# Optimization experiments

Hardware: AMD Instinct MI355X
Metric: run time of the kernel (lower is better)

## Reference

```python
import jax, jax.numpy as jnp
import numpy as np

N, D, H, E = 4096, 256, 8, 131072
HD = D // H
EPS = 1e-5


def layernorm(x, g, b):
    mu = jnp.mean(x, axis=-1, keepdims=True)
    var = jnp.mean((x - mu) ** 2, axis=-1, keepdims=True)
    return (x - mu) * jax.lax.rsqrt(var + EPS) * g + b


def setup_inputs() -> dict:
    key = jax.random.key(0)
    ks = jax.random.split(key, 20)
    s = 1.0 / np.sqrt(D)
    x = jax.random.normal(ks[0], (N, D), jnp.float32)
    adj = jax.random.uniform(ks[1], (N, N)) < 0.01
    adj_mask = adj | jnp.eye(N, dtype=bool)  # self-loops keep softmax rows finite
    edge_index = jax.random.randint(ks[2], (2, E), 0, N, dtype=jnp.int64)
    edge_attr = jax.random.normal(ks[3], (E, D), jnp.float32)
    p = {
        'wq': jax.random.normal(ks[4], (D, D)) * s, 'bq': jnp.zeros((D,)),
        'wk': jax.random.normal(ks[5], (D, D)) * s, 'bk': jnp.zeros((D,)),
        'wv': jax.random.normal(ks[6], (D, D)) * s, 'bv': jnp.zeros((D,)),
        'wo': jax.random.normal(ks[7], (D, D)) * s, 'bo': jnp.zeros((D,)),
        'we': jax.random.normal(ks[8], (D, H)) * s, 'be': jnp.zeros((H,)),
        'w1': jax.random.normal(ks[9], (D, 4 * D)) * s, 'b1': jnp.zeros((4 * D,)),
        'w2': jax.random.normal(ks[10], (4 * D, D)) * (1.0 / np.sqrt(4 * D)), 'b2': jnp.zeros((D,)),
        'g1': jnp.ones((D,)), 'beta1': jnp.zeros((D,)),
        'g2': jnp.ones((D,)), 'beta2': jnp.zeros((D,)),
    }
    return dict(x=x, adj_mask=adj_mask, edge_index=edge_index, edge_attr=edge_attr, **p)


def reference(x, adj_mask, edge_index, edge_attr, wq, bq, wk, bk, wv, bv, wo, bo,
              we, be, w1, b1, w2, b2, g1, beta1, g2, beta2):
    n = x.shape[0]
    Q = (x @ wq + bq).reshape(n, H, HD)
    K = (x @ wk + bk).reshape(n, H, HD)
    V = (x @ wv + bv).reshape(n, H, HD)
    scores = jnp.einsum('nhd,mhd->nmh', Q, K) / np.sqrt(HD)  # [N,N,H]
    edge_bias = edge_attr @ we + be                          # [E,H]
    scores = scores.at[edge_index[0], edge_index[1]].add(edge_bias)
    s = jnp.transpose(scores, (0, 2, 1))                     # [N,H,N]
    s = jnp.where(adj_mask[:, None, :], s, -jnp.inf)
    attn = jax.nn.softmax(s, axis=-1)                        # dropout eval-mode no-op
    ctx = jnp.einsum('nhm,mhd->nhd', attn, V).reshape(n, D)
    attn_out = ctx @ wo + bo
    x1 = layernorm(x + attn_out, g1, beta1)
    ff = jax.nn.gelu(x1 @ w1 + b1, approximate=False) @ w2 + b2
    return layernorm(x1 + ff, g2, beta2)
```

## Files before the change

### kernel.cpp

```cpp
#include <hip/hip_runtime.h>
#include <math.h>

#define NN   4096
#define DD   256
#define HH   8
#define HD   32
#define DFF  1024
#define QKVW 768
#define AC   128
#define EC   128
#define SCPAD 129
#define QSP  36
#define NPB  2

typedef unsigned short ushort_t;
typedef __attribute__((ext_vector_type(8))) short short8;
typedef __attribute__((ext_vector_type(4))) float f32x4;

__device__ __forceinline__ float bf2f(unsigned short u){
  union { unsigned int i; float f; } v; v.i = ((unsigned int)u) << 16; return v.f;
}
__device__ __forceinline__ unsigned short f2bf(float f){
  union { float f; unsigned int i; } v; v.f = f;
  unsigned int x = v.i;
  return (unsigned short)((x + 0x7FFFu + ((x >> 16) & 1u)) >> 16);
}
__device__ __forceinline__ float ldf(const void* p, size_t i, int isbf){
  return isbf ? bf2f(((const ushort_t*)p)[i]) : ((const float*)p)[i];
}
__device__ __forceinline__ ushort_t ldb16(const void* p, size_t i, int isbf){
  return isbf ? ((const ushort_t*)p)[i] : f2bf(((const float*)p)[i]);
}

__global__ void k_detect(const int* __restrict__ adj32, const int* __restrict__ ei32,
                         const unsigned int* __restrict__ g1w, int* __restrict__ flags,
                         int* __restrict__ counts, int* __restrict__ cursor){
  __shared__ int c0s, c1s;
  int t = threadIdx.x;
  if (t == 0) { c0s = 0; c1s = 0; }
  __syncthreads();
  int c0 = 0, c1 = 0;
  for (int i = t; i < 960; i += 256) if (adj32[(size_t)i * 4097] != 0) c0++;
  for (int i = t; i < 2048; i += 256) if (ei32[2*i + 1] != 0) c1++;
  atomicAdd(&c0s, c0); atomicAdd(&c1s, c1);
  for (int i = t; i < NN; i += 256) { counts[i] = 0; cursor[i] = 0; }
  __syncthreads();
  if (t == 0) {
    flags[0] = (c0s == 960) ? 1 : 0;
    flags[1] = (c1s > 100) ? 1 : 0;
    flags[2] = (g1w[0] == 0x3F803F80u) ? 1 : 0;
  }
}

__global__ __launch_bounds__(256) void k_csr(const void* __restrict__ adj,
                                             const int* __restrict__ flags,
                                             int* __restrict__ alist,
                                             int* __restrict__ acnt){
  __shared__ int cntS;
  __shared__ int actS[AC];
  const int n = blockIdx.x, t = threadIdx.x;
  if (t == 0) cntS = 0;
  __syncthreads();
  if (flags[0]) {
    const uint4* arow = (const uint4*)((const int*)adj + (size_t)n * NN);
    #pragma unroll
    for (int i = 0; i < 4; i++) {
      uint4 v = arow[t + 256 * i];
      int c0 = 4 * (t + 256 * i);
      if (v.x) { int p = atomicAdd(&cntS, 1); if (p < AC) actS[p] = c0; }
      if (v.y) { int p = atomicAdd(&cntS, 1); if (p < AC) actS[p] = c0 + 1; }
      if (v.z) { int p = atomicAdd(&cntS, 1); if (p < AC) actS[p] = c0 + 2; }
      if (v.w) { int p = atomicAdd(&cntS, 1); if (p < AC) actS[p] = c0 + 3; }
    }
  } else {
    const uint4* arow = (const uint4*)((const unsigned char*)adj + (size_t)n * NN);
    uint4 v = arow[t];
    unsigned int wsv[4] = {v.x, v.y, v.z, v.w};
    #pragma unroll
    for (int q = 0; q < 4; q++) {
      unsigned int u = wsv[q];
      int c0 = 16 * t + 4 * q;
      if (u & 0x000000FFu) { int p = atomicAdd(&cntS, 1); if (p < AC) actS[p] = c0; }
      if (u & 0x0000FF00u) { int p = atomicAdd(&cntS, 1); if (p < AC) actS[p] = c0 + 1; }
      if (u & 0x00FF0000u) { int p = atomicAdd(&cntS, 1); if (p < AC) actS[p] = c0 + 2; }
      if (u & 0xFF000000u) { int p = atomicAdd(&cntS, 1); if (p < AC) actS[p] = c0 + 3; }
    }
  }
  __syncthreads();
  int m = cntS; if (m > AC) m = AC;
  if (t == 0) acnt[n] = m;
  for (int j = t; j < m; j += 256) alist[(size_t)n * AC + j] = actS[j];
}

#define NX    (NN * DD)
#define NWE   (DD * HH)
#define TPREP 768
__global__ __launch_bounds__(256) void k_prep(
    const void* __restrict__ x, const void* __restrict__ wq, const void* __restrict__ wk,
    const void* __restrict__ wv, const void* __restrict__ wo, const void* __restrict__ w1,
    const void* __restrict__ w2, const void* __restrict__ we,
    const void* __restrict__ bq, const void* __restrict__ bk, const void* __restrict__ bv,
    const void* __restrict__ bo, const void* __restrict__ be, const void* __restrict__ b1,
    const void* __restrict__ b2, const void* __restrict__ g1, const void* __restrict__ be1,
    const void* __restrict__ g2, const void* __restrict__ be2,
    const int* __restrict__ ei, const int* __restrict__ flags,
    ushort_t* __restrict__ xb,
    ushort_t* __restrict__ wqkvT, ushort_t* __restrict__ woT,
    ushort_t* __restrict__ w1T, ushort_t* __restrict__ w2T,
    float* __restrict__ wef, float* __restrict__ bqkvf,
    float* __restrict__ bof, float* __restrict__ bef,
    float* __restrict__ b1f, float* __restrict__ b2f,
    float* __restrict__ g1f, float* __restrict__ be1f,
    float* __restrict__ g2f, float* __restrict__ be2f,
    int* __restrict__ counts, int E, int TOT)
{
  const int isbf = flags[2];
  const int t = threadIdx.x;
  if (blockIdx.x < TPREP) {
    __shared__ ushort_t tile[32][36];
    int b = blockIdx.x;
    const void* src; ushort_t* dst; int R, C, ti;
    if (b < 64)       { src = wq; dst = wqkvT;              R = 256;  C = 256;  ti = b; }
    else if (b < 128) { src = wk; dst = wqkvT + 256 * 256;  R = 256;  C = 256;  ti = b - 64; }
    else if (b < 192) { src = wv; dst = wqkvT + 512 * 256;  R = 256;  C = 256;  ti = b - 128; }
    else if (b < 256) { src = wo; dst = woT;                R = 256;  C = 256;  ti = b - 192; }
    else if (b < 512) { src = w1; dst = w1T;                R = 256;  C = 1024; ti = b - 256; }
    else              { src = w2; dst = w2T;                R = 1024; C = 256;  ti = b - 512; }
    int tiles_c = C >> 5;
    int tr = ti / tiles_c, tc = ti - tr * tiles_c;
    int lr = t >> 3, lc0 = (t & 7) << 2;
    size_t sbase = (size_t)(tr * 32 + lr) * C + tc * 32 + lc0;
    if (isbf) {
      const ushort_t* s16 = (const ushort_t*)src + sbase;
      tile[lr][lc0+0] = s16[0]; tile[lr][lc0+1] = s16[1];
      tile[lr][lc0+2] = s16[2]; tile[lr][lc0+3] = s16[3];
    } else {
      const float4* sf = (const float4*)((const float*)src + sbase);
      float4 v = *sf;
      tile[lr][lc0+0] = f2bf(v.x); tile[lr][lc0+1] = f2bf(v.y);
      tile[lr][lc0+2] = f2bf(v.z); tile[lr][lc0+3] = f2bf(v.w);
    }
    __syncthreads();
    int i = t >> 3, j0 = (t & 7) << 2;
    ushort_t* dp = dst + (size_t)(tc * 32 + i) * R + tr * 32 + j0;
    ushort_t o0 = tile[j0][i], o1 = tile[j0+1][i], o2 = tile[j0+2][i], o3 = tile[j0+3][i];
    dp[0] = o0; dp[1] = o1; dp[2] = o2; dp[3] = o3;
    return;
  }
  const int ei32 = flags[1];
  const int stride = (gridDim.x - TPREP) * 256;
  for (int i = (blockIdx.x - TPREP) * 256 + t; i < TOT; i += stride) {
    int r = i;
    if (r < NX) { xb[r] = ldb16(x, r, isbf); continue; }
    r -= NX;
    if (r < E) {
      int src = ei32 ? ei[r] : ei[2 * r];
      if ((unsigned)src < (unsigned)NN) atomicAdd(&counts[src], 1);
      continue;
    }
    r -= E;
    if (r < NWE) { wef[r] = ldf(we, r, isbf); continue; }
    r -= NWE;
    if (r < QKVW) {
      const void* bs = (r < 256) ? bq : (r < 512) ? bk : bv;
      bqkvf[r] = ldf(bs, r & 255, isbf);
      continue;
    }
    r -= QKVW;
    if (r < DD)  { bof[r] = ldf(bo, r, isbf); continue; }   r -= DD;
    if (r < HH)  { bef[r] = ldf(be, r, isbf); continue; }   r -= HH;
    if (r < DFF) { b1f[r] = ldf(b1, r, isbf); continue; }   r -= DFF;
    if (r < DD)  { b2f[r] = ldf(b2, r, isbf); continue; }   r -= DD;
    if (r < DD)  { g1f[r] = ldf(g1, r, isbf); continue; }   r -= DD;
    if (r < DD)  { be1f[r] = ldf(be1, r, isbf); continue; } r -= DD;
    if (r < DD)  { g2f[r] = ldf(g2, r, isbf); continue; }   r -= DD;
    if (r < DD)  { be2f[r] = ldf(be2, r, isbf); }
  }
}

#define LDK 72
template<int BM>
__global__ __launch_bounds__(256) void k_gemm(
    const ushort_t* __restrict__ A, const ushort_t* __restrict__ Bt,
    const float* __restrict__ bias, void* __restrict__ C,
    int M, int Nn, int K, int act, int mode,
    float* __restrict__ qf, ushort_t* __restrict__ kbuf, ushort_t* __restrict__ vbuf)
{
  constexpr int NF = (BM == 64) ? 2 : 1;
  constexpr int CW = (BM == 64) ? 32 : 16;
  __shared__ ushort_t As[BM * LDK];
  __shared__ ushort_t Bs[64 * LDK];
  const int t = threadIdx.x;
  const int wave = t >> 6, lane = t & 63;
  const int l15 = lane & 15, quad = lane >> 4;
  const int wr = (BM == 64) ? (wave >> 1) : 0;
  const int wc = (BM == 64) ? (wave & 1) : wave;
  const int bm0 = blockIdx.y * BM, bn0 = blockIdx.x * 64;

  const int arow = (BM == 64) ? (t >> 2) : (t >> 3);
  const int akg  = (BM == 64) ? ((t & 3) << 4) : ((t & 7) << 3);
  const int brow = t >> 2, bkg = (t & 3) << 4;

  f32x4 acc[2][NF] = {};

  const ushort_t* ap = A  + (size_t)(bm0 + arow) * K + akg;
  const ushort_t* bp = Bt + (size_t)(bn0 + brow) * K + bkg;
  uint4 a0 = *(const uint4*)ap;
  uint4 a1{};
  if constexpr (BM == 64) a1 = *(const uint4*)(ap + 8);
  uint4 b0 = *(const uint4*)bp;
  uint4 b1 = *(const uint4*)(bp + 8);

  for (int k0 = 0; k0 < K; k0 += 64) {
    __syncthreads();
    *(uint4*)(&As[arow * LDK + akg]) = a0;
    if constexpr (BM == 64) *(uint4*)(&As[arow * LDK + akg + 8]) = a1;
    *(uint4*)(&Bs[brow * LDK + bkg]) = b0;
    *(uint4*)(&Bs[brow * LDK + bkg + 8]) = b1;
    __syncthreads();
    if (k0 + 64 < K) {
      a0 = *(const uint4*)(ap + k0 + 64);
      if constexpr (BM == 64) a1 = *(const uint4*)(ap + k0 + 64 + 8);
      b0 = *(const uint4*)(bp + k0 + 64);
      b1 = *(const uint4*)(bp + k0 + 64 + 8);
    }
    #pragma unroll
    for (int kk = 0; kk < 2; kk++) {
      short8 af[2], bf[NF];
      #pragma unroll
      for (int fr = 0; fr < 2; fr++)
        af[fr] = *(const short8*)(&As[(wr * 32 + fr * 16 + l15) * LDK + kk * 32 + quad * 8]);
      #pragma unroll
      for (int fc = 0; fc < NF; fc++)
        bf[fc] = *(const short8*)(&Bs[(wc * CW + fc * 16 + l15) * LDK + kk * 32 + quad * 8]);
      #pragma unroll
      for (int fr = 0; fr < 2; fr++)
        #pragma unroll
        for (int fc = 0; fc < NF; fc++)
          acc[fr][fc] = __builtin_amdgcn_mfma_f32_16x16x32_bf16(af[fr], bf[fc], acc[fr][fc], 0, 0, 0);
    }
  }

  #pragma unroll
  for (int fr = 0; fr < 2; fr++) {
    #pragma unroll
    for (int fc = 0; fc < NF; fc++) {
      int gn = bn0 + wc * CW + fc * 16 + l15;
      float bcol = bias[gn];
      #pragma unroll
      for (int r = 0; r < 4; r++) {
        int gm = bm0 + wr * 32 + fr * 16 + quad * 4 + r;
        float v = acc[fr][fc][r] + bcol;
        if (act) v = 0.5f * v * (1.0f + erff(v * 0.70710678118654752f));
        if (mode == 2) {
          if (gn < 256)      qf[(size_t)gm * 256 + gn] = v;
          else if (gn < 512) kbuf[(size_t)gm * 256 + (gn - 256)] = f2bf(v);
          else               vbuf[(size_t)gm * 256 + (gn - 512)] = f2bf(v);
        } else if (mode == 1) {
          ((ushort_t*)C)[(size_t)gm * Nn + gn] = f2bf(v);
        } else {
          ((float*)C)[(size_t)gm * Nn + gn] = v;
        }
      }
    }
  }
}

__global__ __launch_bounds__(256) void k_scan(const int* __restrict__ counts,
                                              int* __restrict__ off){
  __shared__ int wsum[4];
  const int t = threadIdx.x, lid = t & 63, wid = t >> 6;
  int loc[16]; int s = 0;
  #pragma unroll
  for (int j = 0; j < 16; j++) { loc[j] = counts[t * 16 + j]; s += loc[j]; }
  const int tot = s;
  #pragma unroll
  for (int o = 1; o < 64; o <<= 1) {
    int u = __shfl_up(s, o, 64);
    if (lid >= o) s += u;
  }
  if (lid == 63) wsum[wid] = s;
  __syncthreads();
  int pre = 0;
  #pragma unroll
  for (int w = 0; w < 4; w++) if (w < wid) pre += wsum[w];
  int run = pre + s - tot;
  if (t == 0) off[0] = 0;
  #pragma unroll
  for (int j = 0; j < 16; j++) { run += loc[j]; off[t * 16 + j + 1] = run; }
}

__global__ void k_scatter(const int* __restrict__ ei, const int* __restrict__ flags,
                          const int* __restrict__ off, int* __restrict__ cursor,
                          int* __restrict__ sdst, int* __restrict__ seid, int e){
  int i = blockIdx.x * 256 + threadIdx.x;
  if (i >= e) return;
  int src, dst;
  if (flags[1]) { src = ei[i];     dst = ei[e + i]; }
  else          { src = ei[2 * i]; dst = ei[2 * (e + i)]; }
  if ((unsigned)src >= (unsigned)NN) return;
  if ((unsigned)dst >= (unsigned)NN) dst = 0;
  int pos = off[src] + atomicAdd(&cursor[src], 1);
  sdst[pos] = dst; seid[pos] = i;
}

__global__ __launch_bounds__(256) void k_ebias(
    const void* __restrict__ ea, const float* __restrict__ wef,
    const float* __restrict__ bef, float* __restrict__ sbias,
    int E, const int* __restrict__ flags)
{
  __shared__ float wel[HH * DD];
  int t = threadIdx.x;
  #pragma unroll
  for (int j = 0; j < 8; j++) wel[j * DD + t] = wef[t * 8 + j];
  const int isbf = flags[2];
  __syncthreads();
  int idx = blockIdx.x * 256 + t;
  int e = idx >> 3, p = idx & 7;
  float acc[8] = {};
  if (e < E) {
    if (isbf) {
      const uint4* base = (const uint4*)((const ushort_t*)ea + (size_t)e * DD);
      #pragma unroll
      for (int q = 0; q < 4; q++) {
        uint4 u = base[q * 8 + p];
        int dbase = 64 * q + 8 * p;
        float f[8];
        union { unsigned int i; float f; } cv;
        cv.i = u.x << 16; f[0] = cv.f; cv.i = u.x & 0xFFFF0000u; f[1] = cv.f;
        cv.i = u.y << 16; f[2] = cv.f; cv.i = u.y & 0xFFFF0000u; f[3] = cv.f;
        cv.i = u.z << 16; f[4] = cv.f; cv.i = u.z & 0xFFFF0000u; f[5] = cv.f;
        cv.i = u.w << 16; f[6] = cv.f; cv.i = u.w & 0xFFFF0000u; f[7] = cv.f;
        #pragma unroll
        for (int j = 0; j < 8; j++)
          #pragma unroll
          for (int h = 0; h < 8; h++)
            acc[h] = fmaf(f[j], wel[h * DD + dbase + j], acc[h]);
      }
    } else {
      const float4* base = (const float4*)((const float*)ea + (size_t)e * DD);
      #pragma unroll
      for (int q = 0; q < 8; q++) {
        float4 u = base[q * 8 + p];
        int dbase = 32 * q + 4 * p;
        #pragma unroll
        for (int h = 0; h < 8; h++) {
          acc[h] = fmaf(u.x, wel[h * DD + dbase + 0], acc[h]);
          acc[h] = fmaf(u.y, wel[h * DD + dbase + 1], acc[h]);
          acc[h] = fmaf(u.z, wel[h * DD + dbase + 2], acc[h]);
          acc[h] = fmaf(u.w, wel[h * DD + dbase + 3], acc[h]);
        }
      }
    }
  }
  #pragma unroll
  for (int h = 0; h < 8; h++) {
    acc[h] += __shfl_xor(acc[h], 1, 8);
    acc[h] += __shfl_xor(acc[h], 2, 8);
    acc[h] += __shfl_xor(acc[h], 4, 8);
  }
  if (e < E) sbias[(size_t)e * 8 + p] = acc[p] + bef[p];
}

__global__ __launch_bounds__(256) void k_attn(
    const float* __restrict__ qf, const ushort_t* __restrict__ kb,
    const ushort_t* __restrict__ vb,
    const int* __restrict__ alist, const int* __restrict__ acnt,
    const int* __restrict__ off, const int* __restrict__ sdst,
    const int* __restrict__ seid, const float* __restrict__ sbias,
    ushort_t* __restrict__ ctxb)
{
  __shared__ float qs[NPB][HH * QSP];
  __shared__ int   act[NPB][AC];
  __shared__ float sc[NPB][HH][SCPAD];
  __shared__ int   edst[NPB][EC];
  __shared__ float ivs[NPB][HH];

  const int t = threadIdx.x;
  const int n0 = blockIdx.x * NPB;

  int na[NPB], cn[NPB], st[NPB];
  #pragma unroll
  for (int s = 0; s < NPB; s++) {
    int n = n0 + s;
    qs[s][(t >> 5) * QSP + (t & 31)] = qf[(size_t)n * DD + t];
    na[s] = min(acnt[n], AC);
    st[s] = off[n];
    int c = off[n + 1] - st[s];
    cn[s] = c < 0 ? 0 : (c > EC ? EC : c);
    for (int j = t; j < na[s]; j += 256) act[s][j] = alist[(size_t)n * AC + j];
    for (int j = t; j < cn[s]; j += 256) edst[s][j] = sdst[st[s] + j];
  }
  __syncthreads();

  #pragma unroll
  for (int s = 0; s < NPB; s++) {
    for (int item = t; item < na[s] * HH; item += 256) {
      int idx = item >> 3, h = item & 7;
      int m = act[s][idx];
      const uint4* kr = (const uint4*)(kb + (size_t)m * DD + h * HD);
      const float* qh = qs[s] + h * QSP;
      float a = 0.f;
      #pragma unroll
      for (int q4 = 0; q4 < 4; q4++) {
        uint4 u = kr[q4];
        int b = q4 * 8;
        union { unsigned int i; float f; } cv;
        cv.i = u.x << 16;         a = fmaf(cv.f, qh[b+0], a);
        cv.i = u.x & 0xFFFF0000u; a = fmaf(cv.f, qh[b+1], a);
        cv.i = u.y << 16;         a = fmaf(cv.f, qh[b+2], a);
        cv.i = u.y & 0xFFFF0000u; a = fmaf(cv.f, qh[b+3], a);
        cv.i = u.z << 16;         a = fmaf(cv.f, qh[b+4], a);
        cv.i = u.z & 0xFFFF0000u; a = fmaf(cv.f, qh[b+5], a);
        cv.i = u.w << 16;         a = fmaf(cv.f, qh[b+6], a);
        cv.i = u.w & 0xFFFF0000u; a = fmaf(cv.f, qh[b+7], a);
      }
      sc[s][h][idx] = a * 0.17677669529663687f;
    }
  }
  __syncthreads();

  #pragma unroll
  for (int s = 0; s < NPB; s++) {
    for (int item = t; item < cn[s] * HH; item += 256) {
      int j = item >> 3, h = item & 7;
      int sid = seid[st[s] + j];
      int dst = edst[s][j];
      int pos = -1;
      for (int i = 0; i < na[s]; i++) if (act[s][i] == dst) { pos = i; break; }
      if (pos >= 0) atomicAdd(&sc[s][h][pos], sbias[(size_t)sid * 8 + h]);
    }
  }
  __syncthreads();

  #pragma unroll
  for (int s = 0; s < NPB; s++) {
    const int h = t >> 5, l = t & 31;
    float lm = -1e30f;
    for (int i = l; i < na[s]; i += 32) lm = fmaxf(lm, sc[s][h][i]);
    #pragma unroll
    for (int o = 16; o > 0; o >>= 1) lm = fmaxf(lm, __shfl_down(lm, o, 32));
    lm = __shfl(lm, 0, 32);
    float ls = 0.f;
    for (int i = l; i < na[s]; i += 32) {
      float e = __expf(sc[s][h][i] - lm);
      sc[s][h][i] = e;
      ls += e;
    }
    #pragma unroll
    for (int o = 16; o > 0; o >>= 1) ls += __shfl_down(ls, o, 32);
    if (l == 0) ivs[s][h] = 1.0f / ls;
  }
  __syncthreads();

  {
    const int s_ = t >> 7, h = (t >> 4) & 7, dp = t & 15;
    const int n_a = s_ ? na[1] : na[0];
    const ushort_t* vcol = vb + h * HD + 2 * dp;
    const float* scp = sc[s_][h];
    float a0 = 0.f, a1 = 0.f;
    int i = 0;
    for (; i + 8 <= n_a; i += 8) {
      int mm[8]; unsigned int vv[8];
      #pragma unroll
      for (int u = 0; u < 8; u++) mm[u] = act[s_][i + u];
      #pragma unroll
      for (int u = 0; u < 8; u++) vv[u] = *(const unsigned int*)(vcol + (size_t)mm[u] * DD);
      #pragma unroll
      for (int u = 0; u < 8; u++) {
        float p = scp[i + u];
        a0 = fmaf(p, bf2f((ushort_t)(vv[u] & 0xFFFFu)), a0);
        a1 = fmaf(p, bf2f((ushort_t)(vv[u] >> 16)), a1);
      }
    }
    for (; i < n_a; i++) {
      unsigned int v = *(const unsigned int*)(vcol + (size_t)act[s_][i] * DD);
      float p = scp[i];
      a0 = fmaf(p, bf2f((ushort_t)(v & 0xFFFFu)), a0);
      a1 = fmaf(p, bf2f((ushort_t)(v >> 16)), a1);
    }
    float iv = ivs[s_][h];
    unsigned int ob = ((unsigned int)f2bf(a1 * iv) << 16) | (unsigned int)f2bf(a0 * iv);
    *(unsigned int*)(ctxb + (size_t)(n0 + s_) * DD + h * HD + 2 * dp) = ob;
  }
}

__global__ __launch_bounds__(256) void k_ln(
    const void* __restrict__ a, const float* __restrict__ b,
    const float* __restrict__ g, const float* __restrict__ beta,
    void* __restrict__ out, ushort_t* __restrict__ out_b,
    int a_raw, int final_mode, const int* __restrict__ flags)
{
  __shared__ float rw[4];
  __shared__ float mu_s, var_s;
  const int n = blockIdx.x, t = threadIdx.x;
  const int wid = t >> 6, lid = t & 63;
  float av = a_raw ? ldf(a, (size_t)n * DD + t, flags[2])
                   : ((const float*)a)[(size_t)n * DD + t];
  float v = av + b[(size_t)n * DD + t];
  float s = v;
  #pragma unroll
  for (int o = 32; o > 0; o >>= 1) s += __shfl_down(s, o, 64);
  if (lid == 0) rw[wid] = s;
  __syncthreads();
  if (t == 0) mu_s = (rw[0] + rw[1] + rw[2] + rw[3]) * (1.0f / 256.0f);
  __syncthreads();
  const float mu = mu_s;
  const float dv = v - mu;
  float q = dv * dv;
  #pragma unroll
  for (int o = 32; o > 0; o >>= 1) q += __shfl_down(q, o, 64);
  if (lid == 0) rw[wid] = q;
  __syncthreads();
  if (t == 0) var_s = (rw[0] + rw[1] + rw[2] + rw[3]) * (1.0f / 256.0f);
  __syncthreads();
  float res = dv * rsqrtf(var_s + 1e-5f) * g[t] + beta[t];
  if (final_mode && flags[2])
    ((ushort_t*)out)[(size_t)n * DD + t] = f2bf(res);
  else
    ((float*)out)[(size_t)n * DD + t] = res;
  if (out_b) out_b[(size_t)n * DD + t] = f2bf(res);
}

extern "C" void kernel_launch(void* const* d_in, const int* in_sizes, int n_in,
                              void* d_out, int out_size, void* d_ws, size_t ws_size,
                              hipStream_t stream)
{
  const void* x   = d_in[0];
  const void* adj = d_in[1];
  const int*  ei  = (const int*)d_in[2];
  const void* ea  = d_in[3];
  const void* wq  = d_in[4];  const void* bq  = d_in[5];
  const void* wk  = d_in[6];  const void* bk  = d_in[7];
  const void* wv  = d_in[8];  const void* bv  = d_in[9];
  const void* wo  = d_in[10]; const void* bo  = d_in[11];
  const void* we  = d_in[12]; const void* be  = d_in[13];
  const void* w1  = d_in[14]; const void* b1  = d_in[15];
  const void* w2  = d_in[16]; const void* b2  = d_in[17];
  const void* g1  = d_in[18]; const void* be1 = d_in[19];
  const void* g2  = d_in[20]; const void* be2 = d_in[21];
  const int E = in_sizes[2] / 2;

  char* w = (char*)d_ws;
  size_t o = 0;
  auto carve = [&](size_t bytes) -> void* {
    void* p = w + o; o = (o + bytes + 255) & ~(size_t)255; return p;
  };
  ushort_t* xb    = (ushort_t*)carve((size_t)NN * DD * 2);
  float*    qfb   = (float*)   carve((size_t)NN * DD * 4);
  ushort_t* kbuf  = (ushort_t*)carve((size_t)NN * DD * 2);
  ushort_t* vbuf  = (ushort_t*)carve((size_t)NN * DD * 2);
  ushort_t* wqkvT = (ushort_t*)carve((size_t)QKVW * DD * 2);
  float*    bqkvf = (float*)   carve(QKVW * 4);
  ushort_t* woT   = (ushort_t*)carve((size_t)DD * DD * 2);
  ushort_t* w1T   = (ushort_t*)carve((size_t)DFF * DD * 2);
  ushort_t* w2T   = (ushort_t*)carve((size_t)DD * DFF * 2);
  float*    wef   = (float*)   carve((size_t)DD * HH * 4);
  float*    bof   = (float*)   carve(DD * 4);
  float*    bef   = (float*)   carve(HH * 4);
  float*    b1f   = (float*)   carve(DFF * 4);
  float*    b2f   = (float*)   carve(DD * 4);
  float*    g1f   = (float*)   carve(DD * 4);
  float*    be1f  = (float*)   carve(DD * 4);
  float*    g2f   = (float*)   carve(DD * 4);
  float*    be2f  = (float*)   carve(DD * 4);
  int*      counts = (int*)carve((size_t)NN * 4);
  int*      cursor = (int*)carve((size_t)NN * 4);
  int*      off    = (int*)carve((size_t)(NN + 1) * 4);
  int*      sdst   = (int*)carve((size_t)E * 4);
  int*      seid   = (int*)carve((size_t)E * 4);
  float*    sbias  = (float*)carve((size_t)E * HH * 4);
  int*      alist  = (int*)carve((size_t)NN * AC * 4);
  int*      acnt   = (int*)carve((size_t)NN * 4);
  ushort_t* ctxb     = (ushort_t*)carve((size_t)NN * DD * 2);
  float*    attn_out = (float*)   carve((size_t)NN * DD * 4);
  float*    x1f      = (float*)   carve((size_t)NN * DD * 4);
  ushort_t* x1b      = (ushort_t*)carve((size_t)NN * DD * 2);
  ushort_t* hbufb    = (ushort_t*)carve((size_t)NN * DFF * 2);
  float*    ff2o     = (float*)   carve((size_t)NN * DD * 4);
  int*      flags    = (int*)carve(4 * 4);

  k_detect<<<1, 256, 0, stream>>>((const int*)adj, ei, (const unsigned int*)g1,
                                  flags, counts, cursor);
  k_csr<<<NN, 256, 0, stream>>>(adj, flags, alist, acnt);

  const int TOT = NX + E + NWE + QKVW + DD + HH + DFF + DD + DD + DD + DD + DD;
  k_prep<<<TPREP + 1280, 256, 0, stream>>>(
      x, wq, wk, wv, wo, w1, w2, we, bq, bk, bv, bo, be, b1, b2,
      g1, be1, g2, be2, ei, flags,
      xb, wqkvT, woT, w1T, w2T, wef, bqkvf,
      bof, bef, b1f, b2f, g1f, be1f, g2f, be2f, counts, E, TOT);

  k_scan<<<1, 256, 0, stream>>>(counts, off);
  int eb = (E + 255) / 256;
  k_scatter<<<eb, 256, 0, stream>>>(ei, flags, off, cursor, sdst, seid, E);
  k_ebias<<<(E * 8 + 255) / 256, 256, 0, stream>>>(ea, wef, bef, sbias, E, flags);

  k_gemm<64><<<dim3(QKVW / 64, NN / 64), 256, 0, stream>>>(
      xb, wqkvT, bqkvf, nullptr, NN, QKVW, DD, 0, 2, qfb, kbuf, vbuf);

  k_attn<<<NN / NPB, 256, 0, stream>>>(qfb, kbuf, vbuf, alist, acnt, off, sdst,
                                       seid, sbias, ctxb);

  k_gemm<32><<<dim3(DD / 64, NN / 32), 256, 0, stream>>>(
      ctxb, woT, bof, attn_out, NN, DD, DD, 0, 0, nullptr, nullptr, nullptr);
  k_ln<<<NN, 256, 0, stream>>>(x, attn_out, g1f, be1f, x1f, x1b, 1, 0, flags);
  k_gemm<64><<<dim3(DFF / 64, NN / 64), 256, 0, stream>>>(
      x1b, w1T, b1f, hbufb, NN, DFF, DD, 1, 1, nullptr, nullptr, nullptr);
  k_gemm<32><<<dim3(DD / 64, NN / 32), 256, 0, stream>>>(
      hbufb, w2T, b2f, ff2o, NN, DD, DFF, 0, 0, nullptr, nullptr, nullptr);
  k_ln<<<NN, 256, 0, stream>>>(x1f, ff2o, g2f, be2f, d_out, (ushort_t*)nullptr, 0, 1, flags);
}
```

Baseline: 419.3 us.

## Fuse output-projection and FFN2 GEMMs with residual LayerNorm; merge scatter into ebias

Adds a k_gemmln kernel in which each block computes a full 16x256 row tile of the GEMM and then applies bias, residual add and LayerNorm in registers. This removes the fp32 attn_out and ff2o intermediates and the separate k_ln launches. The k_scatter CSR fill is folded into k_ebias, with the first 32 threads of each block doing the atomic placement, saving one more launch. In exchange, each k_gemmln block reloads the whole 256-column weight tile and only 256 blocks run, so occupancy and weight reuse per block are lower.

Measured after the change: 410.1 us. -2.2%, faster.

```diff
diff --git a/kernel.cpp b/kernel.cpp
--- a/kernel.cpp
+++ b/kernel.cpp
@@ -179,64 +179,57 @@
 }
 
 #define LDK 72
-template<int BM>
 __global__ __launch_bounds__(256) void k_gemm(
     const ushort_t* __restrict__ A, const ushort_t* __restrict__ Bt,
     const float* __restrict__ bias, void* __restrict__ C,
     int M, int Nn, int K, int act, int mode,
     float* __restrict__ qf, ushort_t* __restrict__ kbuf, ushort_t* __restrict__ vbuf)
 {
-  constexpr int NF = (BM == 64) ? 2 : 1;
-  constexpr int CW = (BM == 64) ? 32 : 16;
-  __shared__ ushort_t As[BM * LDK];
+  __shared__ ushort_t As[64 * LDK];
   __shared__ ushort_t Bs[64 * LDK];
   const int t = threadIdx.x;
   const int wave = t >> 6, lane = t & 63;
   const int l15 = lane & 15, quad = lane >> 4;
-  const int wr = (BM == 64) ? (wave >> 1) : 0;
-  const int wc = (BM == 64) ? (wave & 1) : wave;
-  const int bm0 = blockIdx.y * BM, bn0 = blockIdx.x * 64;
-
-  const int arow = (BM == 64) ? (t >> 2) : (t >> 3);
-  const int akg  = (BM == 64) ? ((t & 3) << 4) : ((t & 7) << 3);
-  const int brow = t >> 2, bkg = (t & 3) << 4;
-
-  f32x4 acc[2][NF] = {};
+  const int wr = wave >> 1, wc = wave & 1;
+  const int bm0 = blockIdx.y * 64, bn0 = blockIdx.x * 64;
+
+  const int arow = t >> 2, akg = (t & 3) << 4;
+
+  f32x4 acc[2][2] = {};
 
   const ushort_t* ap = A  + (size_t)(bm0 + arow) * K + akg;
-  const ushort_t* bp = Bt + (size_t)(bn0 + brow) * K + bkg;
+  const ushort_t* bp = Bt + (size_t)(bn0 + arow) * K + akg;
   uint4 a0 = *(const uint4*)ap;
-  uint4 a1{};
-  if constexpr (BM == 64) a1 = *(const uint4*)(ap + 8);
+  uint4 a1 = *(const uint4*)(ap + 8);
   uint4 b0 = *(const uint4*)bp;
   uint4 b1 = *(const uint4*)(bp + 8);
 
   for (int k0 = 0; k0 < K; k0 += 64) {
     __syncthreads();
     *(uint4*)(&As[arow * LDK + akg]) = a0;
-    if constexpr (BM == 64) *(uint4*)(&As[arow * LDK + akg + 8]) = a1;
-    *(uint4*)(&Bs[brow * LDK + bkg]) = b0;
-    *(uint4*)(&Bs[brow * LDK + bkg + 8]) = b1;
+    *(uint4*)(&As[arow * LDK + akg + 8]) = a1;
+    *(uint4*)(&Bs[arow * LDK + akg]) = b0;
+    *(uint4*)(&Bs[arow * LDK + akg + 8]) = b1;
     __syncthreads();
     if (k0 + 64 < K) {
       a0 = *(const uint4*)(ap + k0 + 64);
-      if constexpr (BM == 64) a1 = *(const uint4*)(ap + k0 + 64 + 8);
+      a1 = *(const uint4*)(ap + k0 + 64 + 8);
       b0 = *(const uint4*)(bp + k0 + 64);
       b1 = *(const uint4*)(bp + k0 + 64 + 8);
     }
     #pragma unroll
     for (int kk = 0; kk < 2; kk++) {
-      short8 af[2], bf[NF];
+      short8 af[2], bf[2];
       #pragma unroll
       for (int fr = 0; fr < 2; fr++)
         af[fr] = *(const short8*)(&As[(wr * 32 + fr * 16 + l15) * LDK + kk * 32 + quad * 8]);
       #pragma unroll
-      for (int fc = 0; fc < NF; fc++)
-        bf[fc] = *(const short8*)(&Bs[(wc * CW + fc * 16 + l15) * LDK + kk * 32 + quad * 8]);
+      for (int fc = 0; fc < 2; fc++)
+        bf[fc] = *(const short8*)(&Bs[(wc * 32 + fc * 16 + l15) * LDK + kk * 32 + quad * 8]);
       #pragma unroll
       for (int fr = 0; fr < 2; fr++)
         #pragma unroll
-        for (int fc = 0; fc < NF; fc++)
+        for (int fc = 0; fc < 2; fc++)
           acc[fr][fc] = __builtin_amdgcn_mfma_f32_16x16x32_bf16(af[fr], bf[fc], acc[fr][fc], 0, 0, 0);
     }
   }
@@ -244,8 +237,8 @@
   #pragma unroll
   for (int fr = 0; fr < 2; fr++) {
     #pragma unroll
-    for (int fc = 0; fc < NF; fc++) {
-      int gn = bn0 + wc * CW + fc * 16 + l15;
+    for (int fc = 0; fc < 2; fc++) {
+      int gn = bn0 + wc * 32 + fc * 16 + l15;
       float bcol = bias[gn];
       #pragma unroll
       for (int r = 0; r < 4; r++) {
@@ -256,11 +249,140 @@
           if (gn < 256)      qf[(size_t)gm * 256 + gn] = v;
           else if (gn < 512) kbuf[(size_t)gm * 256 + (gn - 256)] = f2bf(v);
           else               vbuf[(size_t)gm * 256 + (gn - 512)] = f2bf(v);
-        } else if (mode == 1) {
+        } else {
           ((ushort_t*)C)[(size_t)gm * Nn + gn] = f2bf(v);
-        } else {
-          ((float*)C)[(size_t)gm * Nn + gn] = v;
         }
+      }
+    }
+  }
+}
+
+__global__ __launch_bounds__(512) void k_gemmln(
+    const ushort_t* __restrict__ A, const ushort_t* __restrict__ Bt,
+    const float* __restrict__ bias, const void* __restrict__ res, int res_raw,
+    void* __restrict__ outf, ushort_t* __restrict__ outb,
+    const float* __restrict__ g, const float* __restrict__ beta,
+    int final_mode, const int* __restrict__ flags, int K)
+{
+  __shared__ ushort_t As[16 * LDK];
+  __shared__ ushort_t Bs[256 * LDK];
+  __shared__ float p1[16][8];
+  __shared__ float p2[16][8];
+  const int t = threadIdx.x;
+  const int wave = t >> 6, lane = t & 63;
+  const int l15 = lane & 15, quad = lane >> 4;
+  const int bm0 = blockIdx.x * 16;
+
+  const int arow = t >> 3, akg = (t & 7) << 3;
+  const int brow = t >> 1, bkg = (t & 1) << 5;
+
+  f32x4 acc[2] = {};
+
+  const ushort_t* ap = A + (size_t)(bm0 + arow) * K + akg;
+  const ushort_t* bp = Bt + (size_t)brow * K + bkg;
+  uint4 a0{};
+  if (t < 128) a0 = *(const uint4*)ap;
+  uint4 b0 = *(const uint4*)bp;
+  uint4 b1 = *(const uint4*)(bp + 8);
+  uint4 b2 = *(const uint4*)(bp + 16);
+  uint4 b3 = *(const uint4*)(bp + 24);
+
+  for (int k0 = 0; k0 < K; k0 += 64) {
+    __syncthreads();
+    if (t < 128) *(uint4*)(&As[arow * LDK + akg]) = a0;
+    *(uint4*)(&Bs[brow * LDK + bkg])      = b0;
+    *(uint4*)(&Bs[brow * LDK + bkg + 8])  = b1;
+    *(uint4*)(&Bs[brow * LDK + bkg + 16]) = b2;
+    *(uint4*)(&Bs[brow * LDK + bkg + 24]) = b3;
+    __syncthreads();
+    if (k0 + 64 < K) {
+      if (t < 128) a0 = *(const uint4*)(ap + k0 + 64);
+      b0 = *(const uint4*)(bp + k0 + 64);
+      b1 = *(const uint4*)(bp + k0 + 64 + 8);
+      b2 = *(const uint4*)(bp + k0 + 64 + 16);
+      b3 = *(const uint4*)(bp + k0 + 64 + 24);
+    }
+    #pragma unroll
+    for (int kk = 0; kk < 2; kk++) {
+      short8 af  = *(const short8*)(&As[l15 * LDK + kk * 32 + quad * 8]);
+      short8 bf0 = *(const short8*)(&Bs[(wave * 32 +      l15) * LDK + kk * 32 + quad * 8]);
+      short8 bf1 = *(const short8*)(&Bs[(wave * 32 + 16 + l15) * LDK + kk * 32 + quad * 8]);
+      acc[0] = __builtin_amdgcn_mfma_f32_16x16x32_bf16(af, bf0, acc[0], 0, 0, 0);
+      acc[1] = __builtin_amdgcn_mfma_f32_16x16x32_bf16(af, bf1, acc[1], 0, 0, 0);
+    }
+  }
+
+  const int isbf = flags[2];
+  float v[2][4];
+  #pragma unroll
+  for (int fc = 0; fc < 2; fc++) {
+    int gn = wave * 32 + fc * 16 + l15;
+    float bc = bias[gn];
+    #pragma unroll
+    for (int r = 0; r < 4; r++) {
+      int gm = bm0 + quad * 4 + r;
+      float rv = res_raw ? ldf(res, (size_t)gm * DD + gn, isbf)
+                         : ((const float*)res)[(size_t)gm * DD + gn];
+      v[fc][r] = acc[fc][r] + bc + rv;
+    }
+  }
+  float s1[4];
+  #pragma unroll
+  for (int r = 0; r < 4; r++) {
+    s1[r] = v[0][r] + v[1][r];
+    #pragma unroll
+    for (int o = 1; o < 16; o <<= 1) s1[r] += __shfl_xor(s1[r], o, 64);
+  }
+  if (l15 == 0) {
+    #pragma unroll
+    for (int r = 0; r < 4; r++) p1[quad * 4 + r][wave] = s1[r];
+  }
+  __syncthreads();
+  float mu[4];
+  #pragma unroll
+  for (int r = 0; r < 4; r++) {
+    float m = 0.f;
+    #pragma unroll
+    for (int w = 0; w < 8; w++) m += p1[quad * 4 + r][w];
+    mu[r] = m * (1.0f / 256.0f);
+  }
+  float s2[4];
+  #pragma unroll
+  for (int r = 0; r < 4; r++) {
+    float d0 = v[0][r] - mu[r], d1 = v[1][r] - mu[r];
+    s2[r] = d0 * d0 + d1 * d1;
+    #pragma unroll
+    for (int o = 1; o < 16; o <<= 1) s2[r] += __shfl_xor(s2[r], o, 64);
+  }
+  if (l15 == 0) {
+    #pragma unroll
+    for (int r = 0; r < 4; r++) p2[quad * 4 + r][wave] = s2[r];
+  }
+  __syncthreads();
+  float rs[4];
+  #pragma unroll
+  for (int r = 0; r < 4; r++) {
+    float q = 0.f;
+    #pragma unroll
+    for (int w = 0; w < 8; w++) q += p2[quad * 4 + r][w];
+    rs[r] = rsqrtf(q * (1.0f / 256.0f) + 1e-5f);
+  }
+  #pragma unroll
+  for (int fc = 0; fc < 2; fc++) {
+    int gn = wave * 32 + fc * 16 + l15;
+    float gv = g[gn], bv = beta[gn];
+    #pragma unroll
+    for (int r = 0; r < 4; r++) {
+      int gm = bm0 + quad * 4 + r;
+      float res_v = (v[fc][r] - mu[r]) * rs[r] * gv + bv;
+      if (outb) {
+        ((float*)outf)[(size_t)gm * DD + gn] = res_v;
+        outb[(size_t)gm * DD + gn] = f2bf(res_v);
+      } else {
+        if (final_mode && isbf)
+          ((ushort_t*)outf)[(size_t)gm * DD + gn] = f2bf(res_v);
+        else
+          ((float*)outf)[(size_t)gm * DD + gn] = res_v;
       }
     }
   }
@@ -290,30 +412,31 @@
   for (int j = 0; j < 16; j++) { run += loc[j]; off[t * 16 + j + 1] = run; }
 }
 
-__global__ void k_scatter(const int* __restrict__ ei, const int* __restrict__ flags,
-                          const int* __restrict__ off, int* __restrict__ cursor,
-                          int* __restrict__ sdst, int* __restrict__ seid, int e){
-  int i = blockIdx.x * 256 + threadIdx.x;
-  if (i >= e) return;
-  int src, dst;
-  if (flags[1]) { src = ei[i];     dst = ei[e + i]; }
-  else          { src = ei[2 * i]; dst = ei[2 * (e + i)]; }
-  if ((unsigned)src >= (unsigned)NN) return;
-  if ((unsigned)dst >= (unsigned)NN) dst = 0;
-  int pos = off[src] + atomicAdd(&cursor[src], 1);
-  sdst[pos] = dst; seid[pos] = i;
-}
-
 __global__ __launch_bounds__(256) void k_ebias(
     const void* __restrict__ ea, const float* __restrict__ wef,
     const float* __restrict__ bef, float* __restrict__ sbias,
-    int E, const int* __restrict__ flags)
+    int E, const int* __restrict__ flags,
+    const int* __restrict__ ei, const int* __restrict__ off,
+    int* __restrict__ cursor, int* __restrict__ sdst, int* __restrict__ seid)
 {
   __shared__ float wel[HH * DD];
   int t = threadIdx.x;
   #pragma unroll
   for (int j = 0; j < 8; j++) wel[j * DD + t] = wef[t * 8 + j];
   const int isbf = flags[2];
+  if (t < 32) {
+    int i = blockIdx.x * 32 + t;
+    if (i < E) {
+      int src, dst;
+      if (flags[1]) { src = ei[i];     dst = ei[E + i]; }
+      else          { src = ei[2 * i]; dst = ei[2 * (E + i)]; }
+      if ((unsigned)src < (unsigned)NN) {
+        if ((unsigned)dst >= (unsigned)NN) dst = 0;
+        int pos = off[src] + atomicAdd(&cursor[src], 1);
+        sdst[pos] = dst; seid[pos] = i;
+      }
+    }
+  }
   __syncthreads();
   int idx = blockIdx.x * 256 + t;
   int e = idx >> 3, p = idx & 7;
@@ -483,43 +606,6 @@
     unsigned int ob = ((unsigned int)f2bf(a1 * iv) << 16) | (unsigned int)f2bf(a0 * iv);
     *(unsigned int*)(ctxb + (size_t)(n0 + s_) * DD + h * HD + 2 * dp) = ob;
   }
-}
-
-__global__ __launch_bounds__(256) void k_ln(
-    const void* __restrict__ a, const float* __restrict__ b,
-    const float* __restrict__ g, const float* __restrict__ beta,
-    void* __restrict__ out, ushort_t* __restrict__ out_b,
-    int a_raw, int final_mode, const int* __restrict__ flags)
-{
-  __shared__ float rw[4];
-  __shared__ float mu_s, var_s;
-  const int n = blockIdx.x, t = threadIdx.x;
-  const int wid = t >> 6, lid = t & 63;
-  float av = a_raw ? ldf(a, (size_t)n * DD + t, flags[2])
-                   : ((const float*)a)[(size_t)n * DD + t];
-  float v = av + b[(size_t)n * DD + t];
-  float s = v;
-  #pragma unroll
-  for (int o = 32; o > 0; o >>= 1) s += __shfl_down(s, o, 64);
-  if (lid == 0) rw[wid] = s;
-  __syncthreads();
-  if (t == 0) mu_s = (rw[0] + rw[1] + rw[2] + rw[3]) * (1.0f / 256.0f);
-  __syncthreads();
-  const float mu = mu_s;
-  const float dv = v - mu;
-  float q = dv * dv;
-  #pragma unroll
-  for (int o = 32; o > 0; o >>= 1) q += __shfl_down(q, o, 64);
-  if (lid == 0) rw[wid] = q;
-  __syncthreads();
-  if (t == 0) var_s = (rw[0] + rw[1] + rw[2] + rw[3]) * (1.0f / 256.0f);
-  __syncthreads();
-  float res = dv * rsqrtf(var_s + 1e-5f) * g[t] + beta[t];
-  if (final_mode && flags[2])
-    ((ushort_t*)out)[(size_t)n * DD + t] = f2bf(res);
-  else
-    ((float*)out)[(size_t)n * DD + t] = res;
-  if (out_b) out_b[(size_t)n * DD + t] = f2bf(res);
 }
 
 extern "C" void kernel_launch(void* const* d_in, const int* in_sizes, int n_in,
@@ -573,11 +659,9 @@
   int*      alist  = (int*)carve((size_t)NN * AC * 4);
   int*      acnt   = (int*)carve((size_t)NN * 4);
   ushort_t* ctxb     = (ushort_t*)carve((size_t)NN * DD * 2);
-  float*    attn_out = (float*)   carve((size_t)NN * DD * 4);
   float*    x1f      = (float*)   carve((size_t)NN * DD * 4);
   ushort_t* x1b      = (ushort_t*)carve((size_t)NN * DD * 2);
   ushort_t* hbufb    = (ushort_t*)carve((size_t)NN * DFF * 2);
-  float*    ff2o     = (float*)   carve((size_t)NN * DD * 4);
   int*      flags    = (int*)carve(4 * 4);
 
   k_detect<<<1, 256, 0, stream>>>((const int*)adj, ei, (const unsigned int*)g1,
@@ -592,22 +676,21 @@
       bof, bef, b1f, b2f, g1f, be1f, g2f, be2f, counts, E, TOT);
 
   k_scan<<<1, 256, 0, stream>>>(counts, off);
-  int eb = (E + 255) / 256;
-  k_scatter<<<eb, 256, 0, stream>>>(ei, flags, off, cursor, sdst, seid, E);
-  k_ebias<<<(E * 8 + 255) / 256, 256, 0, stream>>>(ea, wef, bef, sbias, E, flags);
-
-  k_gemm<64><<<dim3(QKVW / 64, NN / 64), 256, 0, stream>>>(
+  k_ebias<<<(E * 8 + 255) / 256, 256, 0, stream>>>(ea, wef, bef, sbias, E, flags,
+                                                   ei, off, cursor, sdst, seid);
+
+  k_gemm<<<dim3(QKVW / 64, NN / 64), 256, 0, stream>>>(
       xb, wqkvT, bqkvf, nullptr, NN, QKVW, DD, 0, 2, qfb, kbuf, vbuf);
 
   k_attn<<<NN / NPB, 256, 0, stream>>>(qfb, kbuf, vbuf, alist, acnt, off, sdst,
                                        seid, sbias, ctxb);
 
-  k_gemm<32><<<dim3(DD / 64, NN / 32), 256, 0, stream>>>(
-      ctxb, woT, bof, attn_out, NN, DD, DD, 0, 0, nullptr, nullptr, nullptr);
-  k_ln<<<NN, 256, 0, stream>>>(x, attn_out, g1f, be1f, x1f, x1b, 1, 0, flags);
-  k_gemm<64><<<dim3(DFF / 64, NN / 64), 256, 0, stream>>>(
+  k_gemmln<<<NN / 16, 512, 0, stream>>>(
+      ctxb, woT, bof, x, 1, x1f, x1b, g1f, be1f, 0, flags, DD);
+
+  k_gemm<<<dim3(DFF / 64, NN / 64), 256, 0, stream>>>(
       x1b, w1T, b1f, hbufb, NN, DFF, DD, 1, 1, nullptr, nullptr, nullptr);
-  k_gemm<32><<<dim3(DD / 64, NN / 32), 256, 0, stream>>>(
-      hbufb, w2T, b2f, ff2o, NN, DD, DFF, 0, 0, nullptr, nullptr, nullptr);
-  k_ln<<<NN, 256, 0, stream>>>(x1f, ff2o, g2f, be2f, d_out, (ushort_t*)nullptr, 0, 1, flags);
-}
+
+  k_gemmln<<<NN / 16, 512, 0, stream>>>(
+      hbufb, w2T, b2f, x1f, 0, d_out, nullptr, g2f, be2f, 1, flags, DFF);
+}
```
